# Kernel tuning notes

Measured on AMD Instinct MI355X. Metric: run time of the kernel, lower is better.

The kernel has to match this reference:

```python
import jax, jax.numpy as jnp
import numpy as np

O, I = 4096, 4096          # out_features, in_features
N = 8192                   # tokens (batch*seq)
ROW_BS, COL_BS = 1, 4      # block sparsity granularity
ZP_OUT = 0                 # output zero point (int)
QMIN, QMAX = -128.0, 127.0 # qint8 range


def setup_inputs() -> dict:
    key = jax.random.key(0)
    k1, k2, k3, k4 = jax.random.split(key, 4)
    # dequantized fp32 activations
    x = jax.random.normal(k1, (N, I), dtype=jnp.float32)
    # int8 weight values (zero point 0), stored as float32 integers in [-127,127]
    w_q = jnp.round(jnp.clip(jax.random.normal(k2, (O, I), dtype=jnp.float32) * 40.0, QMIN + 1, QMAX))
    bias = jax.random.normal(k3, (O,), dtype=jnp.float32) * 0.1
    block_mask = jax.random.randint(k4, (O // ROW_BS, I // COL_BS), 0, 2, dtype=jnp.int32)
    w_scale = jnp.float32(0.01)   # per-tensor weight scale, weight zp == 0
    out_scale = jnp.float32(0.05) # activation (output) quant scale
    return {"x": x, "w_q": w_q, "bias": bias, "w_scale": w_scale,
            "out_scale": out_scale, "block_mask": block_mask}


def reference(x, w_q, bias, w_scale, out_scale, block_mask):
    # expand block mask to element mask [O, I]
    m = jnp.repeat(jnp.repeat(block_mask, ROW_BS, axis=0), COL_BS, axis=1).astype(w_q.dtype)
    w_eff = w_q * m                                  # masked int8 weight values
    # dequantized GEMM: (x @ W^T) * w_scale + bias
    y = jnp.einsum('ni,oi->no', x, w_eff) * w_scale + bias  # [N, O]
    # quantize output to qint8 (scale=out_scale, zp=ZP_OUT), return dequantized repr
    q = jnp.clip(jnp.round(y / out_scale) + ZP_OUT, QMIN, QMAX)
    return (q - ZP_OUT) * out_scale
```

## Files before the change

### kernel.cpp

```cpp
#include <hip/hip_runtime.h>


#define M_TOK 8192
#define O_FEAT 4096
#define K_FEAT 4096

#define BM 256
#define BN 256
#define BK 64
#define NT (K_FEAT / BK)

#define S_BUF 32768
#define S_MAT 16384
#define S_KH  8192

using f16x8 = __attribute__((ext_vector_type(8))) _Float16;
using f32x4 = __attribute__((ext_vector_type(4))) float;

#define BAR()    asm volatile("s_barrier" ::: "memory")
#define LGKM0()  asm volatile("s_waitcnt lgkmcnt(0)" ::: "memory")
#define VMCNT(n) asm volatile("s_waitcnt vmcnt(" #n ")" ::: "memory")
#define SB0()    __builtin_amdgcn_sched_barrier(0)
#define MFMA16(a, b, c) __builtin_amdgcn_mfma_f32_16x16x32_f16((a), (b), (c), 0, 0, 0)

#define NXBLK (M_TOK * K_FEAT / 8 / 256)

__global__ __launch_bounds__(256) void cvt_kernel(const float* __restrict__ x,
                                                  const float* __restrict__ wq,
                                                  const int* __restrict__ mask,
                                                  _Float16* __restrict__ xf,
                                                  _Float16* __restrict__ wf) {
    const int b = blockIdx.x;
    if (b < NXBLK) {
        size_t i = ((size_t)b * 256 + threadIdx.x) * 8;
        float4 v0 = *reinterpret_cast<const float4*>(x + i);
        float4 v1 = *reinterpret_cast<const float4*>(x + i + 4);
        f16x8 h;
        h[0] = (_Float16)v0.x; h[1] = (_Float16)v0.y;
        h[2] = (_Float16)v0.z; h[3] = (_Float16)v0.w;
        h[4] = (_Float16)v1.x; h[5] = (_Float16)v1.y;
        h[6] = (_Float16)v1.z; h[7] = (_Float16)v1.w;
        *reinterpret_cast<f16x8*>(xf + i) = h;
    } else {
        size_t i = ((size_t)(b - NXBLK) * 256 + threadIdx.x) * 8;
        float4 v0 = *reinterpret_cast<const float4*>(wq + i);
        float4 v1 = *reinterpret_cast<const float4*>(wq + i + 4);
        int2 mv = *reinterpret_cast<const int2*>(mask + i / 4);
        float m0 = mv.x ? 1.0f : 0.0f;
        float m1 = mv.y ? 1.0f : 0.0f;
        f16x8 h;
        h[0] = (_Float16)(v0.x * m0); h[1] = (_Float16)(v0.y * m0);
        h[2] = (_Float16)(v0.z * m0); h[3] = (_Float16)(v0.w * m0);
        h[4] = (_Float16)(v1.x * m1); h[5] = (_Float16)(v1.y * m1);
        h[6] = (_Float16)(v1.z * m1); h[7] = (_Float16)(v1.w * m1);
        *reinterpret_cast<f16x8*>(wf + i) = h;
    }
}

__global__ __launch_bounds__(512, 2) void gemm_kernel(const _Float16* __restrict__ A,
                                                      const _Float16* __restrict__ B,
                                                      const float* __restrict__ bias,
                                                      const float* __restrict__ wsp,
                                                      const float* __restrict__ osp,
                                                      float* __restrict__ C) {
    __shared__ __align__(16) _Float16 smem[2][2][2][BM * 32];
    _Float16* sm = &smem[0][0][0][0];

    const int tid  = threadIdx.x;
    const int lane = tid & 63;
    const int w    = tid >> 6;
    const int wm   = w >> 2;
    const int wn   = w & 3;
    const int lr   = lane & 15;
    const int kq   = lane >> 4;

    const int bm = blockIdx.x >> 4;
    const int bn = blockIdx.x & 15;

    const int sr0  = w * 32 + (lane >> 2);
    const int csrc = ((lane & 3) ^ ((lane >> 3) & 3)) * 8;
    const size_t J1 = (size_t)16 * K_FEAT;

    const _Float16* pA0 = A + (size_t)(bm * BM + sr0) * K_FEAT + csrc;
    const _Float16* pA1 = pA0 + 32;
    const _Float16* pB0 = B + (size_t)(bn * BN + sr0) * K_FEAT + csrc;
    const _Float16* pB1 = pB0 + 32;

    const int dst0 = (w * 128 + lane) * 8;
    const int dst1 = dst0 + 64 * 8;

    auto stg = [&](const _Float16* src, const _Float16* dstp) {
        __builtin_amdgcn_global_load_lds(
            (const __attribute__((address_space(1))) void*)(const void*)src,
            (__attribute__((address_space(3))) void*)(void*)(_Float16*)(uintptr_t)dstp,
            16, 0, 0);
    };

    int offA[4], offB[4];
#pragma unroll
    for (int m = 0; m < 4; ++m) {
        const int r = wm * 128 + m * 16 + lr;
        offA[m] = r * 32 + ((kq ^ ((r >> 1) & 3)) << 3);
    }
#pragma unroll
    for (int n = 0; n < 4; ++n) {
        const int r = wn * 64 + n * 16 + lr;
        offB[n] = r * 32 + ((kq ^ ((r >> 1) & 3)) << 3);
    }
    auto rd = [&](const _Float16* sbuf, int off, int immE) -> f16x8 {
        return *reinterpret_cast<const f16x8*>(sbuf + off + immE);
    };

    f32x4 acc[8][4] = {};
    f16x8 a0[4], a1[4], b0v[4], b1v[4];

    stg(pA0, sm + dst0);                 stg(pA0 + J1, sm + dst1);
    stg(pB0, sm + S_MAT + dst0);         stg(pB0 + J1, sm + S_MAT + dst1);
    stg(pA1, sm + S_KH + dst0);          stg(pA1 + J1, sm + S_KH + dst1);
    stg(pB1, sm + S_MAT + S_KH + dst0);  stg(pB1 + J1, sm + S_MAT + S_KH + dst1);
    pA0 += BK; pA1 += BK; pB0 += BK; pB1 += BK;
    stg(pA0, sm + S_BUF + dst0);                 stg(pA0 + J1, sm + S_BUF + dst1);
    stg(pB0, sm + S_BUF + S_MAT + dst0);         stg(pB0 + J1, sm + S_BUF + S_MAT + dst1);
    stg(pA1, sm + S_BUF + S_KH + dst0);          stg(pA1 + J1, sm + S_BUF + S_KH + dst1);
    stg(pB1, sm + S_BUF + S_MAT + S_KH + dst0);  stg(pB1 + J1, sm + S_BUF + S_MAT + S_KH + dst1);
    pA0 += BK; pA1 += BK; pB0 += BK; pB1 += BK;
    VMCNT(8);
    BAR();
#pragma unroll
    for (int m = 0; m < 4; ++m) a0[m] = rd(sm, offA[m], 0);
#pragma unroll
    for (int n = 0; n < 4; ++n) b0v[n] = rd(sm, offB[n], S_MAT);
    LGKM0();
    BAR();

    for (int s = 0; s < NT; ++s) {
        const _Float16* sb = sm + ((s & 1) ? S_BUF : 0);
        const _Float16* sn = sm + ((s & 1) ? 0 : S_BUF);
        const bool more = (s + 1 < NT);
        const bool stg_ok = (s + 2 < NT);

#pragma unroll
        for (int m = 0; m < 4; ++m) a1[m] = rd(sb, offA[m], 2048);
        b1v[0] = rd(sb, offB[0], S_MAT + S_KH);
        b1v[1] = rd(sb, offB[1], S_MAT + S_KH);
        if (stg_ok) { stg(pB0, sb + S_MAT + dst0); stg(pB0 + J1, sb + S_MAT + dst1); }
        SB0();
        __builtin_amdgcn_s_setprio(1);
#pragma unroll
        for (int m = 0; m < 4; ++m)
#pragma unroll
            for (int n = 0; n < 4; ++n)
                acc[m][n] = MFMA16(a0[m], b0v[n], acc[m][n]);
        __builtin_amdgcn_s_setprio(0);
        SB0(); LGKM0();
        BAR();

#pragma unroll
        for (int m = 0; m < 4; ++m) a0[m] = rd(sb, offA[m], S_KH);
        b1v[2] = rd(sb, offB[2], S_MAT + S_KH);
        b1v[3] = rd(sb, offB[3], S_MAT + S_KH);
        if (stg_ok) { stg(pA0, sb + dst0); stg(pA0 + J1, sb + dst1); }
        SB0();
        __builtin_amdgcn_s_setprio(1);
#pragma unroll
        for (int m = 0; m < 4; ++m)
#pragma unroll
            for (int n = 0; n < 4; ++n)
                acc[4 + m][n] = MFMA16(a1[m], b0v[n], acc[4 + m][n]);
        __builtin_amdgcn_s_setprio(0);
        SB0(); LGKM0();
        if (s >= NT - 2) { VMCNT(0); } else { VMCNT(4); }
        BAR();

#pragma unroll
        for (int m = 0; m < 4; ++m) a1[m] = rd(sb, offA[m], S_KH + 2048);
        if (more) {
            b0v[0] = rd(sn, offB[0], S_MAT);
            b0v[1] = rd(sn, offB[1], S_MAT);
        }
        if (stg_ok) { stg(pB1, sb + S_MAT + S_KH + dst0); stg(pB1 + J1, sb + S_MAT + S_KH + dst1); }
        SB0();
        __builtin_amdgcn_s_setprio(1);
#pragma unroll
        for (int m = 0; m < 4; ++m)
#pragma unroll
            for (int n = 0; n < 4; ++n)
                acc[m][n] = MFMA16(a0[m], b1v[n], acc[m][n]);
        __builtin_amdgcn_s_setprio(0);
        SB0(); LGKM0();
        BAR();

        if (more) {
#pragma unroll
            for (int m = 0; m < 4; ++m) a0[m] = rd(sn, offA[m], 0);
            b0v[2] = rd(sn, offB[2], S_MAT);
            b0v[3] = rd(sn, offB[3], S_MAT);
        }
        if (stg_ok) {
            stg(pA1, sb + S_KH + dst0); stg(pA1 + J1, sb + S_KH + dst1);
        }
        SB0();
        __builtin_amdgcn_s_setprio(1);
#pragma unroll
        for (int m = 0; m < 4; ++m)
#pragma unroll
            for (int n = 0; n < 4; ++n)
                acc[4 + m][n] = MFMA16(a1[m], b1v[n], acc[4 + m][n]);
        __builtin_amdgcn_s_setprio(0);
        SB0(); LGKM0();
        BAR();

        pA0 += BK; pA1 += BK; pB0 += BK; pB1 += BK;
    }

    const float wscale = wsp[0];
    const float oscale = osp[0];
    const int row0 = bm * BM + wm * 128;
    const int col0 = bn * BN + wn * 64;
#pragma unroll
    for (int n = 0; n < 4; ++n) {
        const int col = col0 + n * 16 + lr;
        const float bc = bias[col];
#pragma unroll
        for (int m = 0; m < 8; ++m) {
#pragma unroll
            for (int j = 0; j < 4; ++j) {
                const int row = row0 + m * 16 + kq * 4 + j;
                float y = acc[m][n][j] * wscale + bc;
                float q = rintf(y / oscale);
                q = fminf(fmaxf(q, -128.0f), 127.0f);
                C[(size_t)row * O_FEAT + col] = q * oscale;
            }
        }
    }
}

extern "C" void kernel_launch(void* const* d_in, const int* in_sizes, int n_in,
                              void* d_out, int out_size, void* d_ws, size_t ws_size,
                              hipStream_t stream) {
    const float* x        = (const float*)d_in[0];
    const float* wq       = (const float*)d_in[1];
    const float* bias     = (const float*)d_in[2];
    const float* w_scale  = (const float*)d_in[3];
    const float* out_scale= (const float*)d_in[4];
    const int*   mask     = (const int*)d_in[5];
    float* out = (float*)d_out;

    _Float16* xf = (_Float16*)d_ws;
    _Float16* wf = (_Float16*)((char*)d_ws + (size_t)M_TOK * K_FEAT * 2);

    cvt_kernel<<<NXBLK + (O_FEAT * K_FEAT / 8 / 256), 256, 0, stream>>>(x, wq, mask, xf, wf);

    gemm_kernel<<<dim3((M_TOK / BM) * (O_FEAT / BN)), 512, 0, stream>>>(
        xf, wf, bias, w_scale, out_scale, out);
}
```

Baseline: 293.4 us.

## Halve GEMM block to 4 waves with 128x128 per-wave tiles

The GEMM block drops from 8 waves (2x4, each 128x64) to 4 waves (2x2, each 128x128), so each wave holds a 256-accumulator f32 tile and reads 8 B fragments per phase. Global-to-LDS staging is reworked so each thread issues four loads per pane, and the vmcnt thresholds are adjusted to match. The aim is more MFMA work per LDS read and fewer waves contending at barriers. In exchange, register pressure roughly doubles (256 accumulator VGPRs plus operands), occupancy falls to one block per CU, and each thread carries twice the load-issue work.

```diff
diff --git a/kernel.cpp b/kernel.cpp
--- a/kernel.cpp
+++ b/kernel.cpp
@@ -57,7 +57,7 @@
     }
 }
 
-__global__ __launch_bounds__(512, 2) void gemm_kernel(const _Float16* __restrict__ A,
+__global__ __launch_bounds__(256, 1) void gemm_kernel(const _Float16* __restrict__ A,
                                                       const _Float16* __restrict__ B,
                                                       const float* __restrict__ bias,
                                                       const float* __restrict__ wsp,
@@ -69,67 +69,64 @@
     const int tid  = threadIdx.x;
     const int lane = tid & 63;
     const int w    = tid >> 6;
-    const int wm   = w >> 2;
-    const int wn   = w & 3;
+    const int wm   = w >> 1;
+    const int wn   = w & 1;
     const int lr   = lane & 15;
     const int kq   = lane >> 4;
 
     const int bm = blockIdx.x >> 4;
     const int bn = blockIdx.x & 15;
 
-    const int sr0  = w * 32 + (lane >> 2);
-    const int csrc = ((lane & 3) ^ ((lane >> 3) & 3)) * 8;
-    const size_t J1 = (size_t)16 * K_FEAT;
+    const int sr0  = tid >> 2;
+    const int csrc = ((tid & 3) ^ ((tid >> 3) & 3)) * 8;
+    const size_t J64 = (size_t)64 * K_FEAT;
 
     const _Float16* pA0 = A + (size_t)(bm * BM + sr0) * K_FEAT + csrc;
     const _Float16* pA1 = pA0 + 32;
     const _Float16* pB0 = B + (size_t)(bn * BN + sr0) * K_FEAT + csrc;
     const _Float16* pB1 = pB0 + 32;
 
-    const int dst0 = (w * 128 + lane) * 8;
-    const int dst1 = dst0 + 64 * 8;
-
-    auto stg = [&](const _Float16* src, const _Float16* dstp) {
-        __builtin_amdgcn_global_load_lds(
-            (const __attribute__((address_space(1))) void*)(const void*)src,
-            (__attribute__((address_space(3))) void*)(void*)(_Float16*)(uintptr_t)dstp,
-            16, 0, 0);
+    const int dstT = tid * 8;
+
+    auto stg = [&](const _Float16* src, const _Float16* panep) {
+#pragma unroll
+        for (int j = 0; j < 4; ++j)
+            __builtin_amdgcn_global_load_lds(
+                (const __attribute__((address_space(1))) void*)(const void*)(src + j * J64),
+                (__attribute__((address_space(3))) void*)(void*)(_Float16*)(uintptr_t)(panep + dstT + j * 2048),
+                16, 0, 0);
     };
 
-    int offA[4], offB[4];
+    int offA[4], offB[8];
 #pragma unroll
     for (int m = 0; m < 4; ++m) {
         const int r = wm * 128 + m * 16 + lr;
         offA[m] = r * 32 + ((kq ^ ((r >> 1) & 3)) << 3);
     }
 #pragma unroll
-    for (int n = 0; n < 4; ++n) {
-        const int r = wn * 64 + n * 16 + lr;
+    for (int n = 0; n < 8; ++n) {
+        const int r = wn * 128 + n * 16 + lr;
         offB[n] = r * 32 + ((kq ^ ((r >> 1) & 3)) << 3);
     }
     auto rd = [&](const _Float16* sbuf, int off, int immE) -> f16x8 {
         return *reinterpret_cast<const f16x8*>(sbuf + off + immE);
     };
 
-    f32x4 acc[8][4] = {};
-    f16x8 a0[4], a1[4], b0v[4], b1v[4];
-
-    stg(pA0, sm + dst0);                 stg(pA0 + J1, sm + dst1);
-    stg(pB0, sm + S_MAT + dst0);         stg(pB0 + J1, sm + S_MAT + dst1);
-    stg(pA1, sm + S_KH + dst0);          stg(pA1 + J1, sm + S_KH + dst1);
-    stg(pB1, sm + S_MAT + S_KH + dst0);  stg(pB1 + J1, sm + S_MAT + S_KH + dst1);
+    f32x4 acc[8][8] = {};
+    f16x8 a0[4], a1[4], b0v[8], b1v[8];
+
+    stg(pA0, sm);                 stg(pB0, sm + S_MAT);
+    stg(pA1, sm + S_KH);          stg(pB1, sm + S_MAT + S_KH);
     pA0 += BK; pA1 += BK; pB0 += BK; pB1 += BK;
-    stg(pA0, sm + S_BUF + dst0);                 stg(pA0 + J1, sm + S_BUF + dst1);
-    stg(pB0, sm + S_BUF + S_MAT + dst0);         stg(pB0 + J1, sm + S_BUF + S_MAT + dst1);
-    stg(pA1, sm + S_BUF + S_KH + dst0);          stg(pA1 + J1, sm + S_BUF + S_KH + dst1);
-    stg(pB1, sm + S_BUF + S_MAT + S_KH + dst0);  stg(pB1 + J1, sm + S_BUF + S_MAT + S_KH + dst1);
+    stg(pA0, sm + S_BUF);         stg(pB0, sm + S_BUF + S_MAT);
+    stg(pA1, sm + S_BUF + S_KH);  stg(pB1, sm + S_BUF + S_MAT + S_KH);
     pA0 += BK; pA1 += BK; pB0 += BK; pB1 += BK;
-    VMCNT(8);
+    VMCNT(16);
     BAR();
 #pragma unroll
     for (int m = 0; m < 4; ++m) a0[m] = rd(sm, offA[m], 0);
 #pragma unroll
-    for (int n = 0; n < 4; ++n) b0v[n] = rd(sm, offB[n], S_MAT);
+    for (int n = 0; n < 8; ++n) b0v[n] = rd(sm, offB[n], S_MAT);
     LGKM0();
     BAR();
 
@@ -141,15 +138,15 @@
 
 #pragma unroll
         for (int m = 0; m < 4; ++m) a1[m] = rd(sb, offA[m], 2048);
-        b1v[0] = rd(sb, offB[0], S_MAT + S_KH);
-        b1v[1] = rd(sb, offB[1], S_MAT + S_KH);
-        if (stg_ok) { stg(pB0, sb + S_MAT + dst0); stg(pB0 + J1, sb + S_MAT + dst1); }
-        SB0();
-        __builtin_amdgcn_s_setprio(1);
-#pragma unroll
-        for (int m = 0; m < 4; ++m)
-#pragma unroll
-            for (int n = 0; n < 4; ++n)
+#pragma unroll
+        for (int n = 0; n < 4; ++n) b1v[n] = rd(sb, offB[n], S_MAT + S_KH);
+        if (stg_ok) stg(pB0, sb + S_MAT);
+        SB0();
+        __builtin_amdgcn_s_setprio(1);
+#pragma unroll
+        for (int m = 0; m < 4; ++m)
+#pragma unroll
+            for (int n = 0; n < 8; ++n)
                 acc[m][n] = MFMA16(a0[m], b0v[n], acc[m][n]);
         __builtin_amdgcn_s_setprio(0);
         SB0(); LGKM0();
@@ -157,34 +154,34 @@
 
 #pragma unroll
         for (int m = 0; m < 4; ++m) a0[m] = rd(sb, offA[m], S_KH);
-        b1v[2] = rd(sb, offB[2], S_MAT + S_KH);
-        b1v[3] = rd(sb, offB[3], S_MAT + S_KH);
-        if (stg_ok) { stg(pA0, sb + dst0); stg(pA0 + J1, sb + dst1); }
-        SB0();
-        __builtin_amdgcn_s_setprio(1);
-#pragma unroll
-        for (int m = 0; m < 4; ++m)
-#pragma unroll
-            for (int n = 0; n < 4; ++n)
+#pragma unroll
+        for (int n = 4; n < 8; ++n) b1v[n] = rd(sb, offB[n], S_MAT + S_KH);
+        if (stg_ok) stg(pA0, sb);
+        SB0();
+        __builtin_amdgcn_s_setprio(1);
+#pragma unroll
+        for (int m = 0; m < 4; ++m)
+#pragma unroll
+            for (int n = 0; n < 8; ++n)
                 acc[4 + m][n] = MFMA16(a1[m], b0v[n], acc[4 + m][n]);
         __builtin_amdgcn_s_setprio(0);
         SB0(); LGKM0();
-        if (s >= NT - 2) { VMCNT(0); } else { VMCNT(4); }
+        if (s >= NT - 2) { VMCNT(0); } else { VMCNT(8); }
         BAR();
 
 #pragma unroll
         for (int m = 0; m < 4; ++m) a1[m] = rd(sb, offA[m], S_KH + 2048);
         if (more) {
-            b0v[0] = rd(sn, offB[0], S_MAT);
-            b0v[1] = rd(sn, offB[1], S_MAT);
+#pragma unroll
+            for (int n = 0; n < 4; ++n) b0v[n] = rd(sn, offB[n], S_MAT);
         }
-        if (stg_ok) { stg(pB1, sb + S_MAT + S_KH + dst0); stg(pB1 + J1, sb + S_MAT + S_KH + dst1); }
-        SB0();
-        __builtin_amdgcn_s_setprio(1);
-#pragma unroll
-        for (int m = 0; m < 4; ++m)
-#pragma unroll
-            for (int n = 0; n < 4; ++n)
+        if (stg_ok) stg(pB1, sb + S_MAT + S_KH);
+        SB0();
+        __builtin_amdgcn_s_setprio(1);
+#pragma unroll
+        for (int m = 0; m < 4; ++m)
+#pragma unroll
+            for (int n = 0; n < 8; ++n)
                 acc[m][n] = MFMA16(a0[m], b1v[n], acc[m][n]);
         __builtin_amdgcn_s_setprio(0);
         SB0(); LGKM0();
@@ -193,18 +190,16 @@
         if (more) {
 #pragma unroll
             for (int m = 0; m < 4; ++m) a0[m] = rd(sn, offA[m], 0);
-            b0v[2] = rd(sn, offB[2], S_MAT);
-            b0v[3] = rd(sn, offB[3], S_MAT);
+#pragma unroll
+            for (int n = 4; n < 8; ++n) b0v[n] = rd(sn, offB[n], S_MAT);
         }
-        if (stg_ok) {
-            stg(pA1, sb + S_KH + dst0); stg(pA1 + J1, sb + S_KH + dst1);
-        }
-        SB0();
-        __builtin_amdgcn_s_setprio(1);
-#pragma unroll
-        for (int m = 0; m < 4; ++m)
-#pragma unroll
-            for (int n = 0; n < 4; ++n)
+        if (stg_ok) stg(pA1, sb + S_KH);
+        SB0();
+        __builtin_amdgcn_s_setprio(1);
+#pragma unroll
+        for (int m = 0; m < 4; ++m)
+#pragma unroll
+            for (int n = 0; n < 8; ++n)
                 acc[4 + m][n] = MFMA16(a1[m], b1v[n], acc[4 + m][n]);
         __builtin_amdgcn_s_setprio(0);
         SB0(); LGKM0();
@@ -216,9 +211,9 @@
     const float wscale = wsp[0];
     const float oscale = osp[0];
     const int row0 = bm * BM + wm * 128;
-    const int col0 = bn * BN + wn * 64;
-#pragma unroll
-    for (int n = 0; n < 4; ++n) {
+    const int col0 = bn * BN + wn * 128;
+#pragma unroll
+    for (int n = 0; n < 8; ++n) {
         const int col = col0 + n * 16 + lr;
         const float bc = bias[col];
 #pragma unroll
@@ -251,6 +246,6 @@
 
     cvt_kernel<<<NXBLK + (O_FEAT * K_FEAT / 8 / 256), 256, 0, stream>>>(x, wq, mask, xf, wf);
 
-    gemm_kernel<<<dim3((M_TOK / BM) * (O_FEAT / BN)), 512, 0, stream>>>(
+    gemm_kernel<<<dim3((M_TOK / BM) * (O_FEAT / BN)), 256, 0, stream>>>(
         xf, wf, bias, w_scale, out_scale, out);
 }
```

After: 297.8 us. Within noise of the previous version (+1.5%).
